# Kernel tuning notes

Measured on AMD Instinct MI355X. Metric: run time of the kernel, lower is better.

The kernel has to match this reference:

```python
import jax, jax.numpy as jnp
import numpy as np

B, N, C, T, K = 32, 4096, 768, 1000, 20

def setup_inputs() -> dict:
    key = jax.random.key(0)
    k1, k2, k3, k4 = jax.random.split(key, 4)
    g_feat = jax.random.normal(k1, (B, 1, C), dtype=jnp.float32)
    inp = jax.random.normal(k2, (B, N, C), dtype=jnp.float32)
    tau = jax.random.uniform(k3, (1,), dtype=jnp.float32)
    text_embeddings = jax.random.normal(k4, (T, C), dtype=jnp.float32) * 0.01
    return {"g_feat": g_feat, "input": inp, "tau": tau, "text_embeddings": text_embeddings}


def reference(g_feat, input, tau, text_embeddings):
    feat = input  # [B, N, C]
    # 1x1 conv of global feature against text embeddings -> class logits [B, T]
    vg_logit = jnp.einsum('bc,tc->bt', g_feat[:, 0, :], text_embeddings)
    # top-20 candidate categories per image
    _, indices = jax.lax.top_k(vg_logit, K)              # [B, K]
    agg_text_features = text_embeddings[indices]          # [B, K, C] gather
    # per-pixel logits against the 20 gathered text embeddings
    seg_logit = jnp.exp(tau[0]) * jnp.einsum('bkc,bnc->bkn', agg_text_features, feat)  # [B, K, N]
    # hard (straight-through) softmax over candidate axis (dim=-2)
    y_soft = jax.nn.softmax(seg_logit, axis=-2)
    idx = jnp.argmax(seg_logit, axis=-2)                  # [B, N]
    y_hard = jnp.moveaxis(jax.nn.one_hot(idx, K, dtype=seg_logit.dtype), -1, -2)  # [B, K, N]
    attn = y_hard - jax.lax.stop_gradient(y_soft) + y_soft
    # normalize over pixel axis (assign_eps = 1.0)
    assign_attn = attn / (jnp.sum(attn, axis=-1, keepdims=True) + 1.0)
    # combine: [B, N, K] @ [B, K, C] -> [B, N, C]
    text_grids = jnp.einsum('bkn,bkc->bnc', assign_attn, agg_text_features)
    return text_grids
```

## Files before the change

### kernel.cpp

```cpp
#include <hip/hip_runtime.h>
#include <cfloat>

#define B_ 32
#define N_ 4096
#define C_ 768
#define T_ 1000
#define K_ 20

#define PXB 256
#define PHC 32
#define NPH (C_/PHC)
#define GAP_TH 1e-4f
#define MAXF 16384

typedef float f32x4 __attribute__((ext_vector_type(4)));
typedef int   i32x4 __attribute__((ext_vector_type(4)));
typedef short s16x8 __attribute__((ext_vector_type(8)));

__device__ __forceinline__ unsigned short bf_rne(float x) {
    unsigned u = __float_as_uint(x);
    return (unsigned short)((u + 0x7fffu + ((u >> 16) & 1u)) >> 16);
}

__global__ __launch_bounds__(256) void k1_logits(const float* __restrict__ g_feat,
                                                 const float* __restrict__ text,
                                                 double* __restrict__ logits,
                                                 int* __restrict__ cnt,
                                                 int* __restrict__ flagcnt) {
    int b = blockIdx.x;
    int wid = threadIdx.x >> 6, lane = threadIdx.x & 63;
    int t = blockIdx.y * 4 + wid;
    if (b == 0 && blockIdx.y == 0) {
        for (int i = threadIdx.x; i < B_ * K_; i += 256) cnt[i] = 0;
        if (threadIdx.x == 0) flagcnt[0] = 0;
    }
    const float* g = g_feat + b * C_;
    const float* e = text + t * C_;
    double s = 0.0;
    #pragma unroll
    for (int j = 0; j < 12; ++j) {
        int c = lane + 64 * j;
        s += (double)g[c] * (double)e[c];
    }
    #pragma unroll
    for (int m = 32; m; m >>= 1) s += __shfl_xor(s, m);
    if (lane == 0) logits[b * T_ + t] = s;
}

__global__ __launch_bounds__(256) void k1b_topk(const double* __restrict__ logits,
                                                const float* __restrict__ text,
                                                float* __restrict__ agg,
                                                unsigned short* __restrict__ Ehi,
                                                unsigned short* __restrict__ Elo) {
    __shared__ int ssel[K_];
    int b = blockIdx.x, tid = threadIdx.x, lane = tid & 63;
    if (tid < 64) {
        double v[16];
        #pragma unroll
        for (int j = 0; j < 16; ++j) {
            int t = lane + 64 * j;
            v[j] = (t < T_) ? logits[b * T_ + t] : -DBL_MAX;
        }
        for (int it = 0; it < K_; ++it) {
            double bv = -DBL_MAX; int bi = 0x7fffffff;
            #pragma unroll
            for (int j = 0; j < 16; ++j) {
                int t = lane + 64 * j;
                if (v[j] > bv) { bv = v[j]; bi = t; }
            }
            #pragma unroll
            for (int m = 32; m; m >>= 1) {
                double ov = __shfl_xor(bv, m); int oi = __shfl_xor(bi, m);
                if (ov > bv || (ov == bv && oi < bi)) { bv = ov; bi = oi; }
            }
            if (lane == 0) ssel[it] = bi;
            #pragma unroll
            for (int j = 0; j < 16; ++j) {
                int t = lane + 64 * j;
                if (t == bi) v[j] = -DBL_MAX;
            }
        }
    }
    __syncthreads();
    for (int i = tid; i < K_ * C_; i += 256) {
        int j = i / C_, c = i - j * C_;
        agg[b * K_ * C_ + i] = text[ssel[j] * C_ + c];
    }
    for (int i = tid; i < 32 * C_; i += 256) {
        int r = i / C_, c = i - r * C_;
        float v = (r < K_) ? text[ssel[r] * C_ + c] : 0.f;
        unsigned u = __float_as_uint(v);
        float fh = __uint_as_float(u & 0xffff0000u);
        Ehi[(size_t)b * 32 * C_ + i] = (unsigned short)(u >> 16);
        Elo[(size_t)b * 32 * C_ + i] = bf_rne(v - fh);
    }
}

__global__ __launch_bounds__(256, 2) void k2_argmax(const float* __restrict__ feat,
                                                    const unsigned short* __restrict__ Ehi,
                                                    const unsigned short* __restrict__ Elo,
                                                    int* __restrict__ kidx,
                                                    int* __restrict__ cnt,
                                                    int* __restrict__ flagcnt,
                                                    int* __restrict__ flaglist) {
    __shared__ unsigned short hiT[2][PXB * PHC];
    __shared__ unsigned short loT[2][PXB * PHC];
    __shared__ int scnt[K_];
    int bx = blockIdx.x;
    int b = bx >> 4, tile = bx & 15;
    int n0 = tile * PXB;
    int tid = threadIdx.x, wid = tid >> 6, lane = tid & 63;
    if (tid < K_) scnt[tid] = 0;
    __syncthreads();

    const float* fb = feat + ((size_t)b * N_ + n0) * C_;
    const unsigned short* Eh = Ehi + (size_t)b * 32 * C_;
    const unsigned short* El = Elo + (size_t)b * 32 * C_;
    int r2 = (tid >> 1) & 3;
    int arow = lane & 15, acg = lane >> 4;

    f32x4 fr[8];
    auto LOADF = [&](int p) {
        const f32x4* fp_ = (const f32x4*)(fb + (size_t)tid * C_ + p * PHC);
        #pragma unroll
        for (int q = 0; q < 8; ++q) fr[q] = fp_[q ^ (2 * r2)];
    };
    auto CVTW = [&](int buf) {
        #pragma unroll
        for (int j = 0; j < 4; ++j) {
            unsigned hu[8], lu[8];
            #pragma unroll
            for (int m = 0; m < 8; ++m) {
                float x = (m < 4) ? fr[2 * j][m] : fr[2 * j + 1][m - 4];
                unsigned u = __float_as_uint(x);
                float fh = __uint_as_float(u & 0xffff0000u);
                hu[m] = u >> 16;
                lu[m] = bf_rne(x - fh);
            }
            int slot = tid * 4 + (j ^ r2);
            i32x4 hv = { (int)(hu[0] | (hu[1] << 16)), (int)(hu[2] | (hu[3] << 16)),
                         (int)(hu[4] | (hu[5] << 16)), (int)(hu[6] | (hu[7] << 16)) };
            i32x4 lv = { (int)(lu[0] | (lu[1] << 16)), (int)(lu[2] | (lu[3] << 16)),
                         (int)(lu[4] | (lu[5] << 16)), (int)(lu[6] | (lu[7] << 16)) };
            *(i32x4*)&hiT[buf][slot * 8] = hv;
            *(i32x4*)&loT[buf][slot * 8] = lv;
        }
    };

    s16x8 Ach0, Ach1, Acl0, Acl1, Anh0, Anh1, Anl0, Anl1;
    auto LOADA = [&](int p, s16x8& h0, s16x8& h1, s16x8& l0, s16x8& l1) {
        int co = p * PHC + acg * 8;
        h0 = *(const s16x8*)(Eh + (size_t)arow * C_ + co);
        h1 = *(const s16x8*)(Eh + (size_t)(16 + arow) * C_ + co);
        l0 = *(const s16x8*)(El + (size_t)arow * C_ + co);
        l1 = *(const s16x8*)(El + (size_t)(16 + arow) * C_ + co);
    };

    f32x4 acc0[4], acc1[4];
    #pragma unroll
    for (int i = 0; i < 4; ++i) { acc0[i] = (f32x4)0.f; acc1[i] = (f32x4)0.f; }

    LOADF(0);
    CVTW(0);
    LOADF(1);
    LOADA(0, Ach0, Ach1, Acl0, Acl1);
    LOADA(1, Anh0, Anh1, Anl0, Anl1);
    __syncthreads();

    #pragma unroll 1
    for (int p = 0; p < NPH; ++p) {
        int cur = p & 1;
        if (p + 1 < NPH) {
            CVTW(cur ^ 1);
            if (p + 2 < NPH) LOADF(p + 2);
            asm volatile("s_waitcnt lgkmcnt(0)" ::: "memory");
        }
        asm volatile("s_barrier" ::: "memory");

        #pragma unroll
        for (int i = 0; i < 4; ++i) {
            int slot = (wid * 64 + i * 16 + arow) * 4 + acg;
            s16x8 Bh = *(const s16x8*)&hiT[cur][slot * 8];
            s16x8 Bl = *(const s16x8*)&loT[cur][slot * 8];
            acc0[i] = __builtin_amdgcn_mfma_f32_16x16x32_bf16(Ach0, Bh, acc0[i], 0, 0, 0);
            acc1[i] = __builtin_amdgcn_mfma_f32_16x16x32_bf16(Ach1, Bh, acc1[i], 0, 0, 0);
            acc0[i] = __builtin_amdgcn_mfma_f32_16x16x32_bf16(Ach0, Bl, acc0[i], 0, 0, 0);
            acc1[i] = __builtin_amdgcn_mfma_f32_16x16x32_bf16(Ach1, Bl, acc1[i], 0, 0, 0);
            acc0[i] = __builtin_amdgcn_mfma_f32_16x16x32_bf16(Acl0, Bh, acc0[i], 0, 0, 0);
            acc1[i] = __builtin_amdgcn_mfma_f32_16x16x32_bf16(Acl1, Bh, acc1[i], 0, 0, 0);
        }
        asm volatile("s_barrier" ::: "memory");

        Ach0 = Anh0; Ach1 = Anh1; Acl0 = Anl0; Acl1 = Anl1;
        if (p + 2 < NPH) LOADA(p + 2, Anh0, Anh1, Anl0, Anl1);
    }

    #pragma unroll
    for (int i = 0; i < 4; ++i) {
        int kb = acg * 4;
        float m1 = acc0[i][0]; int i1 = kb; float m2 = -FLT_MAX;
        #pragma unroll
        for (int r = 1; r < 4; ++r) {
            float v = acc0[i][r];
            if (v > m1) { m2 = m1; m1 = v; i1 = kb + r; }
            else if (v > m2) m2 = v;
        }
        if (acg == 0) {
            #pragma unroll
            for (int r = 0; r < 4; ++r) {
                float v = acc1[i][r];
                if (v > m1) { m2 = m1; m1 = v; i1 = 16 + r; }
                else if (v > m2) m2 = v;
            }
        }
        #pragma unroll
        for (int s = 16; s < 64; s <<= 1) {
            float om1 = __shfl_xor(m1, s); int oi1 = __shfl_xor(i1, s);
            float om2 = __shfl_xor(m2, s);
            if (om1 > m1 || (om1 == m1 && oi1 < i1)) { m2 = fmaxf(m1, om2); m1 = om1; i1 = oi1; }
            else { m2 = fmaxf(m2, om1); }
        }
        if (lane < 16) {
            int n = n0 + wid * 64 + i * 16 + lane;
            kidx[b * N_ + n] = i1;
            atomicAdd(&scnt[i1], 1);
            if (m1 - m2 < GAP_TH) {
                int pos = atomicAdd(flagcnt, 1);
                if (pos < MAXF) flaglist[pos] = b * N_ + n;
            }
        }
    }
    __syncthreads();
    if (tid < K_) atomicAdd(&cnt[b * K_ + tid], scnt[tid]);
}

__global__ __launch_bounds__(256) void k25_refine(const float* __restrict__ feat,
                                                  const float* __restrict__ agg,
                                                  int* __restrict__ kidx,
                                                  int* __restrict__ cnt,
                                                  const int* __restrict__ flagcnt,
                                                  const int* __restrict__ flaglist) {
    int wid = threadIdx.x >> 6, lane = threadIdx.x & 63;
    int wg = blockIdx.x * 4 + wid;
    int nf = flagcnt[0]; if (nf > MAXF) nf = MAXF;
    for (int e = wg; e < nf; e += gridDim.x * 4) {
        int pix = flaglist[e];
        int b = pix >> 12;
        const float* fr = feat + (size_t)pix * C_;
        const float* ebase = agg + b * K_ * C_;
        double fd[12];
        #pragma unroll
        for (int j = 0; j < 12; ++j) fd[j] = (double)fr[lane + 64 * j];
        double best = -DBL_MAX; int bi = 0;
        for (int k = 0; k < K_; ++k) {
            const float* er = ebase + k * C_;
            double s = 0.0;
            #pragma unroll
            for (int j = 0; j < 12; ++j) s += fd[j] * (double)er[lane + 64 * j];
            #pragma unroll
            for (int m = 32; m; m >>= 1) s += __shfl_xor(s, m);
            if (s > best) { best = s; bi = k; }
        }
        if (lane == 0) {
            int old = kidx[pix];
            if (old != bi) {
                kidx[pix] = bi;
                atomicSub(&cnt[b * K_ + old], 1);
                atomicAdd(&cnt[b * K_ + bi], 1);
            }
        }
    }
}

__global__ __launch_bounds__(256) void k4_out(const float* __restrict__ agg,
                                              const int* __restrict__ cnt,
                                              const int* __restrict__ kidx,
                                              float* __restrict__ out) {
    int wid = threadIdx.x >> 6, lane = threadIdx.x & 63;
    int wg = blockIdx.x * 4 + wid;
    int base = wg * 8;
    int b = base >> 12;
    int kk[8];
    #pragma unroll
    for (int i = 0; i < 8; ++i) kk[i] = kidx[base + i];
    float sc[8];
    #pragma unroll
    for (int i = 0; i < 8; ++i) sc[i] = 1.0f / ((float)cnt[b * K_ + kk[i]] + 1.0f);
    const f32x4* agg4 = (const f32x4*)agg;
    f32x4* out4 = (f32x4*)out;
    #pragma unroll
    for (int i = 0; i < 8; ++i) {
        const f32x4* a4 = agg4 + (size_t)(b * K_ + kk[i]) * (C_ / 4);
        f32x4* o4 = out4 + (size_t)(base + i) * (C_ / 4);
        #pragma unroll
        for (int j = 0; j < 3; ++j) {
            f32x4 v = a4[lane + 64 * j];
            v *= sc[i];
            o4[lane + 64 * j] = v;
        }
    }
}

extern "C" void kernel_launch(void* const* d_in, const int* in_sizes, int n_in,
                              void* d_out, int out_size, void* d_ws, size_t ws_size,
                              hipStream_t stream) {
    const float* g_feat = (const float*)d_in[0];
    const float* feat   = (const float*)d_in[1];
    const float* text   = (const float*)d_in[3];
    float* out = (float*)d_out;

    char* ws = (char*)d_ws;
    double* logits        = (double*)(ws + 0);
    float*  agg           = (float*) (ws + 262144);
    int*    cnt           = (int*)   (ws + 2230784);
    int*    flagc         = (int*)   (ws + 2233344);
    int*    flagl         = (int*)   (ws + 2233408);
    int*    kidx          = (int*)   (ws + 2301504);
    unsigned short* Ehi   = (unsigned short*)(ws + 2825792);
    unsigned short* Elo   = (unsigned short*)(ws + 4398656);

    k1_logits<<<dim3(32, 250), 256, 0, stream>>>(g_feat, text, logits, cnt, flagc);
    k1b_topk<<<32, 256, 0, stream>>>(logits, text, agg, Ehi, Elo);
    k2_argmax<<<32 * 16, 256, 0, stream>>>(feat, Ehi, Elo, kidx, cnt, flagc, flagl);
    k25_refine<<<1024, 256, 0, stream>>>(feat, agg, kidx, cnt, flagc, flagl);
    k4_out<<<4096, 256, 0, stream>>>(agg, cnt, kidx, out);
}
```

Before: 273.5 us.

## Drop k2 LDS barriers, pre-scale gathered embeddings, prefetch rows in output kernel

The k2 argmax main loop no longer uses the pre-loop __syncthreads or the two s_barriers per phase. It keeps only an lgkmcnt wait and a scheduling barrier, to cut per-phase synchronisation stalls. This is only safe if each wave reads just the LDS slots it wrote itself; otherwise it adds a data race on the double buffer. A new small kernel pre-scales the gathered text embeddings by 1/(count+1). The output kernel then becomes a pure gather-copy that software-prefetches the next row, taking the per-pixel reciprocal and count loads out of the bandwidth-bound write loop.

```diff
diff --git a/kernel.cpp b/kernel.cpp
--- a/kernel.cpp
+++ b/kernel.cpp
@@ -165,7 +165,6 @@
     LOADF(1);
     LOADA(0, Ach0, Ach1, Acl0, Acl1);
     LOADA(1, Anh0, Anh1, Anl0, Anl1);
-    __syncthreads();
 
     #pragma unroll 1
     for (int p = 0; p < NPH; ++p) {
@@ -173,9 +172,9 @@
         if (p + 1 < NPH) {
             CVTW(cur ^ 1);
             if (p + 2 < NPH) LOADF(p + 2);
-            asm volatile("s_waitcnt lgkmcnt(0)" ::: "memory");
-        }
-        asm volatile("s_barrier" ::: "memory");
+        }
+        asm volatile("s_waitcnt lgkmcnt(0)" ::: "memory");
+        __builtin_amdgcn_sched_barrier(0);
 
         #pragma unroll
         for (int i = 0; i < 4; ++i) {
@@ -189,7 +188,6 @@
             acc0[i] = __builtin_amdgcn_mfma_f32_16x16x32_bf16(Acl0, Bh, acc0[i], 0, 0, 0);
             acc1[i] = __builtin_amdgcn_mfma_f32_16x16x32_bf16(Acl1, Bh, acc1[i], 0, 0, 0);
         }
-        asm volatile("s_barrier" ::: "memory");
 
         Ach0 = Anh0; Ach1 = Anh1; Acl0 = Anl0; Acl1 = Anl1;
         if (p + 2 < NPH) LOADA(p + 2, Anh0, Anh1, Anl0, Anl1);
@@ -272,8 +270,23 @@
     }
 }
 
-__global__ __launch_bounds__(256) void k4_out(const float* __restrict__ agg,
-                                              const int* __restrict__ cnt,
+__global__ __launch_bounds__(256) void k3s_scale(const float* __restrict__ agg,
+                                                 const int* __restrict__ cnt,
+                                                 float* __restrict__ sagg) {
+    __shared__ float sc[K_];
+    int b = blockIdx.x, tid = threadIdx.x;
+    if (tid < K_) sc[tid] = 1.0f / ((float)cnt[b * K_ + tid] + 1.0f);
+    __syncthreads();
+    const f32x4* a4 = (const f32x4*)(agg + (size_t)b * K_ * C_);
+    f32x4* s4 = (f32x4*)(sagg + (size_t)b * K_ * C_);
+    #pragma unroll 1
+    for (int i = tid; i < K_ * (C_ / 4); i += 256) {
+        int k = i / (C_ / 4);
+        s4[i] = a4[i] * sc[k];
+    }
+}
+
+__global__ __launch_bounds__(256) void k4_out(const float* __restrict__ sagg,
                                               const int* __restrict__ kidx,
                                               float* __restrict__ out) {
     int wid = threadIdx.x >> 6, lane = threadIdx.x & 63;
@@ -283,21 +296,23 @@
     int kk[8];
     #pragma unroll
     for (int i = 0; i < 8; ++i) kk[i] = kidx[base + i];
-    float sc[8];
-    #pragma unroll
-    for (int i = 0; i < 8; ++i) sc[i] = 1.0f / ((float)cnt[b * K_ + kk[i]] + 1.0f);
-    const f32x4* agg4 = (const f32x4*)agg;
+    const f32x4* sagg4 = (const f32x4*)sagg;
     f32x4* out4 = (f32x4*)out;
+
+    f32x4 va0, va1, va2, vb0, vb1, vb2;
+    {
+        const f32x4* a4 = sagg4 + (size_t)(b * K_ + kk[0]) * (C_ / 4);
+        va0 = a4[lane]; va1 = a4[lane + 64]; va2 = a4[lane + 128];
+    }
     #pragma unroll
     for (int i = 0; i < 8; ++i) {
-        const f32x4* a4 = agg4 + (size_t)(b * K_ + kk[i]) * (C_ / 4);
+        if (i + 1 < 8) {
+            const f32x4* a4 = sagg4 + (size_t)(b * K_ + kk[i + 1]) * (C_ / 4);
+            vb0 = a4[lane]; vb1 = a4[lane + 64]; vb2 = a4[lane + 128];
+        }
         f32x4* o4 = out4 + (size_t)(base + i) * (C_ / 4);
-        #pragma unroll
-        for (int j = 0; j < 3; ++j) {
-            f32x4 v = a4[lane + 64 * j];
-            v *= sc[i];
-            o4[lane + 64 * j] = v;
-        }
+        o4[lane] = va0; o4[lane + 64] = va1; o4[lane + 128] = va2;
+        va0 = vb0; va1 = vb1; va2 = vb2;
     }
 }
 
@@ -318,10 +333,12 @@
     int*    kidx          = (int*)   (ws + 2301504);
     unsigned short* Ehi   = (unsigned short*)(ws + 2825792);
     unsigned short* Elo   = (unsigned short*)(ws + 4398656);
+    float*  sagg          = (float*) (ws + 5971520);
 
     k1_logits<<<dim3(32, 250), 256, 0, stream>>>(g_feat, text, logits, cnt, flagc);
     k1b_topk<<<32, 256, 0, stream>>>(logits, text, agg, Ehi, Elo);
     k2_argmax<<<32 * 16, 256, 0, stream>>>(feat, Ehi, Elo, kidx, cnt, flagc, flagl);
     k25_refine<<<1024, 256, 0, stream>>>(feat, agg, kidx, cnt, flagc, flagl);
-    k4_out<<<4096, 256, 0, stream>>>(agg, cnt, kidx, out);
-}
+    k3s_scale<<<32, 256, 0, stream>>>(agg, cnt, sagg);
+    k4_out<<<4096, 256, 0, stream>>>(sagg, kidx, out);
+}
```

Result: slower. 281.5 us (+2.9%).
